# Kernel optimization log

Measured on AMD Instinct MI355X. Metric: run time of the kernel, lower is better.

Reference implementation:

```python
import jax, jax.numpy as jnp
import numpy as np

N_QUBITS = 10
DEPTH = 6


def _ry(theta):
    # RY(theta) = [[cos(t/2), -sin(t/2)], [sin(t/2), cos(t/2)]]
    c = jnp.cos(theta / 2)
    s = jnp.sin(theta / 2)
    return jnp.stack([jnp.stack([c, -s]), jnp.stack([s, c])]).astype(jnp.complex64)


def _rot(phi, theta, omega):
    # PennyLane Rot(phi, theta, omega) = RZ(omega) RY(theta) RZ(phi)
    c = jnp.cos(theta / 2)
    s = jnp.sin(theta / 2)
    ep = jnp.exp(-0.5j * (phi + omega).astype(jnp.complex64))
    em = jnp.exp(-0.5j * (phi - omega).astype(jnp.complex64))
    return jnp.stack([
        jnp.stack([ep * c, -jnp.conj(em) * s]),
        jnp.stack([em * s, jnp.conj(ep) * c]),
    ])


def _apply_1q(psi, U, w):
    # psi: (2,)*n statevector; apply 2x2 unitary U on qubit axis w
    psi = jnp.tensordot(U, psi, axes=([1], [w]))
    return jnp.moveaxis(psi, 0, w)


def _apply_cnot(psi, c, t):
    # flip target axis t on the control=1 slice of axis c
    psi = jnp.moveaxis(psi, (c, t), (0, 1))
    psi = jnp.concatenate([psi[:1], psi[1:, ::-1]], axis=0)
    return jnp.moveaxis(psi, (0, 1), (c, t))


def _circuit(angles, weights):
    """RY encoding + StronglyEntanglingLayers + PauliZ expvals. angles: (n,), weights: (depth, n, 3)."""
    n = N_QUBITS
    psi = jnp.zeros((2,) * n, jnp.complex64).at[(0,) * n].set(1.0)
    for i in range(n):
        psi = _apply_1q(psi, _ry(angles[i]), i)
    for l in range(DEPTH):
        for i in range(n):
            psi = _apply_1q(psi, _rot(weights[l, i, 0], weights[l, i, 1], weights[l, i, 2]), i)
        r = (l % (n - 1)) + 1  # default StronglyEntanglingLayers range schedule
        for i in range(n):
            psi = _apply_cnot(psi, i, (i + r) % n)
    p = psi.real ** 2 + psi.imag ** 2  # probabilities, shape (2,)*n
    exps = []
    for i in range(n):
        pm = jnp.moveaxis(p, i, 0).reshape(2, -1).sum(axis=1)
        exps.append(pm[0] - pm[1])  # <Z_i>
    return jnp.stack(exps)


def setup_inputs() -> dict:
    key = jax.random.key(0)
    ks = jax.random.split(key, 5)
    B, F, C = 8192, 1024, 10
    x = jax.random.normal(ks[0], (B, F), jnp.float32)
    W_proj = jax.random.normal(ks[1], (N_QUBITS, F), jnp.float32) / np.sqrt(F).astype(np.float32)
    weights = 0.01 * jax.random.normal(ks[2], (DEPTH, N_QUBITS, 3), jnp.float32)
    W_out = jax.random.normal(ks[3], (C, N_QUBITS), jnp.float32) / np.sqrt(N_QUBITS).astype(np.float32)
    b_out = 0.01 * jax.random.normal(ks[4], (C,), jnp.float32)
    return {"x": x, "W_proj": W_proj, "weights": weights, "W_out": W_out, "b_out": b_out}


def reference(x, W_proj, weights, W_out, b_out):
    # classical projection + angle encoding
    angles = jnp.tanh(x @ W_proj.T) * jnp.float32(np.pi / 2)  # (B, n_qubits)
    # batched exact statevector simulation of the VQC
    q = jax.vmap(_circuit, in_axes=(0, None))(angles, weights)  # (B, n_qubits)
    return q @ W_out.T + b_out  # (B, num_classes)
```

## Files before the change

### kernel.cpp

```cpp
#include <hip/hip_runtime.h>
#include <math.h>
#include <stdint.h>

#define NQ 10
#define DEPTH 6

typedef _Float16 f16x8 __attribute__((ext_vector_type(8)));
typedef float f32x4 __attribute__((ext_vector_type(4)));

typedef __attribute__((address_space(3))) unsigned int lds_u32;
typedef const __attribute__((address_space(1))) unsigned int glb_u32;

__device__ __forceinline__ void async_load16(const unsigned short* g, unsigned short* l) {
    __builtin_amdgcn_global_load_lds((glb_u32*)g, (lds_u32*)l, 16, 0, 0);
}

__device__ __forceinline__ void compute_gate(const float* __restrict__ weights,
                                             int idx, float* __restrict__ g) {
    float phi   = weights[idx * 3 + 0];
    float theta = weights[idx * 3 + 1];
    float omega = weights[idx * 3 + 2];
    float c = cosf(0.5f * theta), s = sinf(0.5f * theta);
    float ap = -0.5f * (phi + omega);
    float am = -0.5f * (phi - omega);
    float epr = cosf(ap), epi = sinf(ap);
    float emr = cosf(am), emi = sinf(am);
    g[0] =  epr * c;  g[1] =  epi * c;
    g[2] = -emr * s;  g[3] =  emi * s;
    g[4] =  emr * s;  g[5] =  emi * s;
    g[6] =  epr * c;  g[7] = -epi * c;
}

__global__ void prep_gates_kernel(const float* __restrict__ weights,
                                  float* __restrict__ gmat) {
    int idx = blockIdx.x * blockDim.x + threadIdx.x;
    if (idx >= DEPTH * NQ) return;
    compute_gate(weights, idx, gmat + idx * 8);
}

__device__ __forceinline__ void apply_1q_local(
    float (&ar)[16], float (&ai)[16], int q,
    float u00r, float u00i, float u01r, float u01i,
    float u10r, float u10i, float u11r, float u11i) {
#pragma unroll
    for (int j = 0; j < 16; ++j) {
        if ((j >> q) & 1) continue;
        int j1 = j | (1 << q);
        float a0r = ar[j],  a0i = ai[j];
        float a1r = ar[j1], a1i = ai[j1];
        ar[j]  = u00r*a0r - u00i*a0i + u01r*a1r - u01i*a1i;
        ai[j]  = u00r*a0i + u00i*a0r + u01r*a1i + u01i*a1r;
        ar[j1] = u10r*a0r - u10i*a0i + u11r*a1r - u11i*a1i;
        ai[j1] = u10r*a0i + u10i*a0r + u11r*a1i + u11i*a1r;
    }
}

__device__ __forceinline__ void apply_1q_lane(
    float (&ar)[16], float (&ai)[16], int q, int lane,
    float u00r, float u00i, float u01r, float u01i,
    float u10r, float u10i, float u11r, float u11i) {
    int  m  = 1 << (q - 4);
    bool hi = (lane >> (q - 4)) & 1;
    float car = hi ? u11r : u00r, cai = hi ? u11i : u00i;
    float cbr = hi ? u10r : u01r, cbi = hi ? u10i : u01i;
    float pr[16], pi[16];
#pragma unroll
    for (int j = 0; j < 16; ++j) pr[j] = __shfl_xor(ar[j], m, 64);
#pragma unroll
    for (int j = 0; j < 16; ++j) pi[j] = __shfl_xor(ai[j], m, 64);
#pragma unroll
    for (int j = 0; j < 16; ++j) {
        float mr = ar[j], mi = ai[j];
        ar[j] = car*mr - cai*mi + cbr*pr[j] - cbi*pi[j];
        ai[j] = car*mi + cai*mr + cbr*pi[j] + cbi*pr[j];
    }
}

__device__ __forceinline__ void cnot_gate(
    float (&ar)[16], float (&ai)[16], int c, int t, int lane) {
    if (c < 4 && t < 4) {
#pragma unroll
        for (int j = 0; j < 16; ++j) {
            if (((j >> c) & 1) && !((j >> t) & 1)) {
                int j1 = j | (1 << t);
                float tr = ar[j]; ar[j] = ar[j1]; ar[j1] = tr;
                float ti = ai[j]; ai[j] = ai[j1]; ai[j1] = ti;
            }
        }
    } else if (c < 4) {
        int m = 1 << (t - 4);
        float pr[16], pi[16];
#pragma unroll
        for (int j = 0; j < 16; ++j)
            if ((j >> c) & 1) pr[j] = __shfl_xor(ar[j], m, 64);
#pragma unroll
        for (int j = 0; j < 16; ++j)
            if ((j >> c) & 1) pi[j] = __shfl_xor(ai[j], m, 64);
#pragma unroll
        for (int j = 0; j < 16; ++j)
            if ((j >> c) & 1) { ar[j] = pr[j]; ai[j] = pi[j]; }
    } else if (t < 4) {
        bool cb = (lane >> (c - 4)) & 1;
#pragma unroll
        for (int j = 0; j < 16; ++j) {
            if (!((j >> t) & 1)) {
                int j1 = j | (1 << t);
                float lr = ar[j], li = ai[j], hr = ar[j1], hi2 = ai[j1];
                ar[j]  = cb ? hr : lr;  ai[j]  = cb ? hi2 : li;
                ar[j1] = cb ? lr : hr;  ai[j1] = cb ? li : hi2;
            }
        }
    } else {
        int  m  = 1 << (t - 4);
        bool cb = (lane >> (c - 4)) & 1;
        float pr[16], pi[16];
#pragma unroll
        for (int j = 0; j < 16; ++j) pr[j] = __shfl_xor(ar[j], m, 64);
#pragma unroll
        for (int j = 0; j < 16; ++j) pi[j] = __shfl_xor(ai[j], m, 64);
#pragma unroll
        for (int j = 0; j < 16; ++j) {
            ar[j] = cb ? pr[j] : ar[j];
            ai[j] = cb ? pi[j] : ai[j];
        }
    }
}

template <int R>
__device__ __forceinline__ void cnot_ring(float (&ar)[16], float (&ai)[16], int lane) {
#pragma unroll
    for (int i = 0; i < NQ; ++i) cnot_gate(ar, ai, i, (i + R) % NQ, lane);
}

template <int R>
__device__ __forceinline__ void cnot_ring_rev(float (&ar)[16], float (&ai)[16], int lane) {
#pragma unroll
    for (int i = NQ - 1; i >= 0; --i) cnot_gate(ar, ai, i, (i + R) % NQ, lane);
}

__device__ __forceinline__ void run_circuit(float (&ar)[16], float (&ai)[16],
                                            const float* __restrict__ gmat, int lane) {
    for (int l = 0; l < DEPTH; ++l) {
        const float* gl = gmat + l * (NQ * 8);
#pragma unroll
        for (int i = 0; i < NQ; ++i) {
            const float* g = gl + i * 8;
            float u00r = g[0], u00i = g[1], u01r = g[2], u01i = g[3];
            float u10r = g[4], u10i = g[5], u11r = g[6], u11i = g[7];
            if (i < 4)
                apply_1q_local(ar, ai, i, u00r,u00i,u01r,u01i,u10r,u10i,u11r,u11i);
            else
                apply_1q_lane(ar, ai, i, lane, u00r,u00i,u01r,u01i,u10r,u10i,u11r,u11i);
        }
        switch (l) {
            case 0: cnot_ring<1>(ar, ai, lane); break;
            case 1: cnot_ring<2>(ar, ai, lane); break;
            case 2: cnot_ring<3>(ar, ai, lane); break;
            case 3: cnot_ring<4>(ar, ai, lane); break;
            case 4: cnot_ring<5>(ar, ai, lane); break;
            default: cnot_ring<6>(ar, ai, lane); break;
        }
    }
}

__device__ __forceinline__ void run_circuit_T(float (&ar)[16], float (&ai)[16],
                                              const float* __restrict__ gmat, int lane) {
    for (int l = DEPTH - 1; l >= 0; --l) {
        switch (l) {
            case 0: cnot_ring_rev<1>(ar, ai, lane); break;
            case 1: cnot_ring_rev<2>(ar, ai, lane); break;
            case 2: cnot_ring_rev<3>(ar, ai, lane); break;
            case 3: cnot_ring_rev<4>(ar, ai, lane); break;
            case 4: cnot_ring_rev<5>(ar, ai, lane); break;
            default: cnot_ring_rev<6>(ar, ai, lane); break;
        }
        const float* gl = gmat + l * (NQ * 8);
#pragma unroll
        for (int i = 0; i < NQ; ++i) {
            const float* g = gl + i * 8;
            float u00r = g[0], u00i = g[1];
            float u01r = g[4], u01i = g[5];
            float u10r = g[2], u10i = g[3];
            float u11r = g[6], u11i = g[7];
            if (i < 4)
                apply_1q_local(ar, ai, i, u00r,u00i,u01r,u01i,u10r,u10i,u11r,u11i);
            else
                apply_1q_lane(ar, ai, i, lane, u00r,u00i,u01r,u01i,u10r,u10i,u11r,u11i);
        }
    }
}

__device__ __forceinline__ float wave_sum(float v) {
#pragma unroll
    for (int m = 1; m < 64; m <<= 1) v += __shfl_xor(v, m, 64);
    return v;
}

__device__ __forceinline__ void proj_v_body(
    const float* __restrict__ x, const float* __restrict__ Wproj,
    _Float16* __restrict__ V, int b, int lane) {
    const float4* xb4 = (const float4*)(x + (size_t)b * 1024);
    const float4* W4  = (const float4*)Wproj;
    float acc[NQ];
#pragma unroll
    for (int q = 0; q < NQ; ++q) acc[q] = 0.f;
#pragma unroll
    for (int k4 = 0; k4 < 4; ++k4) {
        float4 xv = xb4[k4 * 64 + lane];
#pragma unroll
        for (int q = 0; q < NQ; ++q) {
            float4 wv = W4[q * 256 + k4 * 64 + lane];
            acc[q] = fmaf(xv.x, wv.x, acc[q]);
            acc[q] = fmaf(xv.y, wv.y, acc[q]);
            acc[q] = fmaf(xv.z, wv.z, acc[q]);
            acc[q] = fmaf(xv.w, wv.w, acc[q]);
        }
    }
#pragma unroll
    for (int q = 0; q < NQ; ++q) acc[q] = wave_sum(acc[q]);

    float cq[NQ], sq[NQ];
#pragma unroll
    for (int q = 0; q < NQ; ++q) {
        float ang = tanhf(acc[q]) * 1.57079632679489662f;
        cq[q] = cosf(0.5f * ang);
        sq[q] = sinf(0.5f * ang);
    }
    float laneprod = 1.f;
#pragma unroll
    for (int q = 4; q < NQ; ++q)
        laneprod *= ((lane >> (q - 4)) & 1) ? sq[q] : cq[q];

    unsigned int buf[8];
#pragma unroll
    for (int jj = 0; jj < 8; ++jj) {
        unsigned short h2[2];
#pragma unroll
        for (int c = 0; c < 2; ++c) {
            int j = jj * 2 + c;
            float p = laneprod;
#pragma unroll
            for (int q = 0; q < 4; ++q) p *= ((j >> q) & 1) ? sq[q] : cq[q];
            h2[c] = __builtin_bit_cast(unsigned short, (_Float16)p);
        }
        buf[jj] = (unsigned int)h2[0] | ((unsigned int)h2[1] << 16);
    }
    uint4* dst = (uint4*)(V + (size_t)b * 1024 + 16 * lane);
    uint4 v0; v0.x = buf[0]; v0.y = buf[1]; v0.z = buf[2]; v0.w = buf[3];
    uint4 v1; v1.x = buf[4]; v1.y = buf[5]; v1.z = buf[6]; v1.w = buf[7];
    dst[0] = v0; dst[1] = v1;
}

__global__ __launch_bounds__(256) void basis_proj_kernel(
    const float* __restrict__ weights, _Float16* __restrict__ Bt,
    const float* __restrict__ x, const float* __restrict__ Wproj,
    _Float16* __restrict__ V, int B) {
    __shared__ float gmat_s[DEPTH * NQ * 8];
    int tid  = threadIdx.x;
    int lane = tid & 63;
    int w    = tid >> 6;

    if (blockIdx.x < 256) {
        if (tid < DEPTH * NQ) compute_gate(weights, tid, gmat_s + tid * 8);
        __syncthreads();

        int g = blockIdx.x * 4 + w;
        float ar[16], ai[16];
#pragma unroll
        for (int jj = 0; jj < 16; ++jj) {
            ar[jj] = (lane == (g >> 4) && jj == (g & 15)) ? 1.f : 0.f;
            ai[jj] = 0.f;
        }
        run_circuit_T(ar, ai, gmat_s, lane);

        unsigned int bufr[8], bufi[8];
#pragma unroll
        for (int jj = 0; jj < 8; ++jj) {
            unsigned short r0 = __builtin_bit_cast(unsigned short, (_Float16)ar[2*jj]);
            unsigned short r1 = __builtin_bit_cast(unsigned short, (_Float16)ar[2*jj+1]);
            unsigned short i0 = __builtin_bit_cast(unsigned short, (_Float16)ai[2*jj]);
            unsigned short i1 = __builtin_bit_cast(unsigned short, (_Float16)ai[2*jj+1]);
            bufr[jj] = (unsigned int)r0 | ((unsigned int)r1 << 16);
            bufi[jj] = (unsigned int)i0 | ((unsigned int)i1 << 16);
        }
        uint4* dre = (uint4*)((unsigned short*)Bt + (size_t)(2*g)     * 1024 + 16 * lane);
        uint4* dim = (uint4*)((unsigned short*)Bt + (size_t)(2*g + 1) * 1024 + 16 * lane);
        uint4 v;
        v.x = bufr[0]; v.y = bufr[1]; v.z = bufr[2]; v.w = bufr[3]; dre[0] = v;
        v.x = bufr[4]; v.y = bufr[5]; v.z = bufr[6]; v.w = bufr[7]; dre[1] = v;
        v.x = bufi[0]; v.y = bufi[1]; v.z = bufi[2]; v.w = bufi[3]; dim[0] = v;
        v.x = bufi[4]; v.y = bufi[5]; v.z = bufi[6]; v.w = bufi[7]; dim[1] = v;
    } else {
        int b = (blockIdx.x - 256) * 4 + w;
        if (b < B) proj_v_body(x, Wproj, V, b, lane);
    }
}

#define STAGE(buf, kt_) do {                                                        \
    unsigned short* As_ = lds_s + (buf) * 32768;                                    \
    unsigned short* Bs_ = As_ + 16384;                                              \
    _Pragma("unroll")                                                               \
    for (int r_ = 0; r_ < 4; ++r_) {                                                \
        int s_   = w * 4 + r_;                                                      \
        int row_ = s_ * 8 + srow;                                                   \
        async_load16(A  + (size_t)(m0 + row_) * 1024 + (kt_) * 64 + schnk * 8,      \
                     As_ + s_ * 512);                                               \
        async_load16(Bt + (size_t)(n0 + row_) * 1024 + (kt_) * 64 + schnk * 8,      \
                     Bs_ + s_ * 512);                                               \
    }                                                                               \
} while (0)

__global__ __launch_bounds__(512, 2) void gemm_fused_kernel(
    const unsigned short* __restrict__ A,
    const unsigned short* __restrict__ Bt,
    float* __restrict__ Zpart) {
    __shared__ __align__(16) unsigned short lds_s[2 * 32768];
    int tid  = threadIdx.x;
    int lane = tid & 63;
    int w    = tid >> 6;
    int wm   = w >> 2;
    int wn   = w & 3;
    int by   = blockIdx.x & 7;
    int bx   = blockIdx.x >> 3;
    int m0   = bx * 256;
    int n0   = by * 256;
    int quad = lane >> 4;
    int lrow = lane & 15;
    int srow  = (lane >> 3);
    int schnk = (lane & 7) ^ srow;

    f32x4 acc[8][4];
#pragma unroll
    for (int mi = 0; mi < 8; ++mi)
#pragma unroll
        for (int ni = 0; ni < 4; ++ni)
            acc[mi][ni] = (f32x4){0.f, 0.f, 0.f, 0.f};

    STAGE(0, 0);

#pragma unroll 2
    for (int kt = 0; kt < 16; ++kt) {
        int cur = kt & 1;
        if (kt < 15) {
            STAGE(cur ^ 1, kt + 1);
            asm volatile("s_waitcnt vmcnt(8)" ::: "memory");
        } else {
            asm volatile("s_waitcnt vmcnt(0)" ::: "memory");
        }
        __builtin_amdgcn_s_barrier();
        asm volatile("" ::: "memory");
        const unsigned short* As_ = lds_s + cur * 32768;
        const unsigned short* Bs_ = As_ + 16384;
#pragma unroll
        for (int kk = 0; kk < 2; ++kk) {
            int cx = (kk * 4 + quad) ^ (lrow & 7);
            f16x8 bf[4];
#pragma unroll
            for (int ni = 0; ni < 4; ++ni)
                bf[ni] = *(const f16x8*)(Bs_ + (wn * 64 + ni * 16 + lrow) * 64 + cx * 8);
            __builtin_amdgcn_s_setprio(1);
#pragma unroll
            for (int mi = 0; mi < 8; ++mi) {
                f16x8 af = *(const f16x8*)(As_ + (wm * 128 + mi * 16 + lrow) * 64 + cx * 8);
#pragma unroll
                for (int ni = 0; ni < 4; ++ni)
                    acc[mi][ni] = __builtin_amdgcn_mfma_f32_16x16x32_f16(
                        af, bf[ni], acc[mi][ni], 0, 0, 0);
            }
            __builtin_amdgcn_s_setprio(0);
        }
        asm volatile("" ::: "memory");
        __builtin_amdgcn_s_barrier();
    }

    float* Zs = (float*)lds_s;
    int nbl  = wn >> 1;
    int half = wn & 1;
#pragma unroll
    for (int mi = 0; mi < 8; ++mi) {
#pragma unroll
        for (int r = 0; r < 4; ++r) {
            float p0 = acc[mi][0][r] * acc[mi][0][r];
            float p1 = acc[mi][1][r] * acc[mi][1][r];
            float p2 = acc[mi][2][r] * acc[mi][2][r];
            float p3 = acc[mi][3][r] * acc[mi][3][r];
            float t0 = (p0 + p1) + (p2 + p3);
            float t3 = (p0 - p1) + (p2 - p3);
            float t4 = (p0 + p1) - (p2 + p3);
            t0 += __shfl_xor(t0, 1, 64);
            t3 += __shfl_xor(t3, 1, 64);
            t4 += __shfl_xor(t4, 1, 64);
            float u2 = __shfl_xor(t0, 2, 64);
            float ap = t0 + u2;
            float am = (lane & 2) ? u2 - t0 : t0 - u2;
            t3 += __shfl_xor(t3, 2, 64);
            t4 += __shfl_xor(t4, 2, 64);
            float u4  = __shfl_xor(ap, 4, 64);
            float bpp = ap + u4;
            float bpm = (lane & 4) ? u4 - ap : ap - u4;
            float bmp = am + __shfl_xor(am, 4, 64);
            t3 += __shfl_xor(t3, 4, 64);
            t4 += __shfl_xor(t4, 4, 64);
            float u8 = __shfl_xor(bpp, 8, 64);
            float T  = bpp + u8;
            float Z2 = (lane & 8) ? u8 - bpp : bpp - u8;
            float Z1 = bpm + __shfl_xor(bpm, 8, 64);
            float Z0 = bmp + __shfl_xor(bmp, 8, 64);
            t3 += __shfl_xor(t3, 8, 64);
            t4 += __shfl_xor(t4, 8, 64);
            if (lrow == 0) {
                int row = wm * 128 + mi * 16 + quad * 4 + r;
                float* z = Zs + ((size_t)(nbl * 2 + half) * 256 + row) * 9;
                z[0] = T;  z[1] = Z0; z[2] = Z1; z[3] = Z2;
                z[4] = t3; z[5] = t4;
            }
        }
    }
    __syncthreads();
    {
        int row  = tid >> 1, part = tid & 1;
#pragma unroll
        for (int nb = 0; nb < 2; ++nb) {
            const float* za = Zs + ((size_t)(nb * 2 + 0) * 256 + row) * 9;
            const float* zb = Zs + ((size_t)(nb * 2 + 1) * 256 + row) * 9;
            float o[4];
            if (part == 0) {
                o[0] = za[0] + zb[0];
                o[1] = za[1] + zb[1];
                o[2] = za[2] + zb[2];
                o[3] = za[3] + zb[3];
            } else {
                o[0] = za[4] + zb[4];
                o[1] = za[5] + zb[5];
                o[2] = za[0] - zb[0];
                o[3] = 0.f;
            }
            float4 v = {o[0], o[1], o[2], o[3]};
            *(float4*)(Zpart + ((size_t)(m0 + row) * 16 + (by * 2 + nb)) * 8 + part * 4) = v;
        }
    }
}

__global__ __launch_bounds__(256) void combine_head_kernel(
    const float* __restrict__ Zpart, const float* __restrict__ Wout,
    const float* __restrict__ bout, float* __restrict__ out, int B) {
    int lane = threadIdx.x & 63;
    int wid  = threadIdx.x >> 6;
    int b    = blockIdx.x * 4 + wid;
    if (b >= B) return;

    float z[8];
    if (lane < 16) {
        const float4* p = (const float4*)(Zpart + ((size_t)b * 16 + lane) * 8);
        float4 a = p[0], c = p[1];
        z[0]=a.x; z[1]=a.y; z[2]=a.z; z[3]=a.w; z[4]=c.x; z[5]=c.y; z[6]=c.z; z[7]=c.w;
    } else {
#pragma unroll
        for (int i = 0; i < 8; ++i) z[i] = 0.f;
    }
    float Zq[NQ];
#pragma unroll
    for (int q = 0; q < 6; ++q) {
        float v = z[q + 1];
        v += __shfl_xor(v, 1, 64);
        v += __shfl_xor(v, 2, 64);
        v += __shfl_xor(v, 4, 64);
        v += __shfl_xor(v, 8, 64);
        Zq[q] = v;
    }
    {
        float T = z[0];
        float u1 = __shfl_xor(T, 1, 64);
        float P  = T + u1;
        float M  = (lane & 1) ? u1 - T : T - u1;
        float u2 = __shfl_xor(P, 2, 64);
        float PP = P + u2;
        float PM = (lane & 2) ? u2 - P : P - u2;
        float MP = M + __shfl_xor(M, 2, 64);
        float u4  = __shfl_xor(PP, 4, 64);
        float PPP = PP + u4;
        float PPM = (lane & 4) ? u4 - PP : PP - u4;
        float PMP = PM + __shfl_xor(PM, 4, 64);
        float MPP = MP + __shfl_xor(MP, 4, 64);
        float u8 = __shfl_xor(PPP, 8, 64);
        Zq[9] = (lane & 8) ? u8 - PPP : PPP - u8;
        Zq[8] = PPM + __shfl_xor(PPM, 8, 64);
        Zq[7] = PMP + __shfl_xor(PMP, 8, 64);
        Zq[6] = MPP + __shfl_xor(MPP, 8, 64);
    }
    if (lane < NQ) {
        float o = bout[lane];
#pragma unroll
        for (int q = 0; q < NQ; ++q) o = fmaf(Zq[q], Wout[lane * NQ + q], o);
        out[(size_t)b * NQ + lane] = o;
    }
}

__global__ __launch_bounds__(256) void vqc_kernel(
    const float* __restrict__ x, const float* __restrict__ Wproj,
    const float* __restrict__ gmat, const float* __restrict__ Wout,
    const float* __restrict__ bout, float* __restrict__ out, int B) {
    int lane = threadIdx.x & 63;
    int wid  = threadIdx.x >> 6;
    int b    = blockIdx.x * 4 + wid;
    if (b >= B) return;

    const float* xb = x + (size_t)b * 1024;
    float acc[NQ];
#pragma unroll
    for (int q = 0; q < NQ; ++q) acc[q] = 0.f;
#pragma unroll
    for (int k = 0; k < 16; ++k) {
        float xv = xb[k * 64 + lane];
#pragma unroll
        for (int q = 0; q < NQ; ++q)
            acc[q] = fmaf(xv, Wproj[q * 1024 + k * 64 + lane], acc[q]);
    }
#pragma unroll
    for (int q = 0; q < NQ; ++q) acc[q] = wave_sum(acc[q]);

    float cq[NQ], sq[NQ];
#pragma unroll
    for (int q = 0; q < NQ; ++q) {
        float ang = tanhf(acc[q]) * 1.57079632679489662f;
        cq[q] = cosf(0.5f * ang);
        sq[q] = sinf(0.5f * ang);
    }
    float laneprod = 1.f;
#pragma unroll
    for (int q = 4; q < NQ; ++q)
        laneprod *= ((lane >> (q - 4)) & 1) ? sq[q] : cq[q];
    float ar[16], ai[16];
#pragma unroll
    for (int j = 0; j < 16; ++j) {
        float p = laneprod;
#pragma unroll
        for (int q = 0; q < 4; ++q) p *= ((j >> q) & 1) ? sq[q] : cq[q];
        ar[j] = p; ai[j] = 0.f;
    }
    run_circuit(ar, ai, gmat, lane);

    float T = 0.f, S[4] = {0.f, 0.f, 0.f, 0.f};
#pragma unroll
    for (int j = 0; j < 16; ++j) {
        float p = ar[j] * ar[j] + ai[j] * ai[j];
        T += p;
#pragma unroll
        for (int q = 0; q < 4; ++q) S[q] += ((j >> q) & 1) ? -p : p;
    }
    float Zq[NQ];
#pragma unroll
    for (int q = 0; q < 4; ++q) Zq[q] = S[q];
#pragma unroll
    for (int q = 4; q < NQ; ++q) Zq[q] = ((lane >> (q - 4)) & 1) ? -T : T;
#pragma unroll
    for (int q = 0; q < NQ; ++q) Zq[q] = wave_sum(Zq[q]);
    if (lane < NQ) {
        float o = bout[lane];
#pragma unroll
        for (int q = 0; q < NQ; ++q) o = fmaf(Zq[q], Wout[lane * NQ + q], o);
        out[(size_t)b * NQ + lane] = o;
    }
}

extern "C" void kernel_launch(void* const* d_in, const int* in_sizes, int n_in,
                              void* d_out, int out_size, void* d_ws, size_t ws_size,
                              hipStream_t stream) {
    const float* x       = (const float*)d_in[0];
    const float* Wproj   = (const float*)d_in[1];
    const float* weights = (const float*)d_in[2];
    const float* Wout    = (const float*)d_in[3];
    const float* bout    = (const float*)d_in[4];
    float* out = (float*)d_out;
    int B = in_sizes[0] / 1024;

    char* ws = (char*)d_ws;
    size_t off_Bt = 4096;
    size_t off_V  = off_Bt + (size_t)2048 * 1024 * 2;
    size_t off_Z  = off_V  + (size_t)B * 1024 * 2;
    size_t need   = off_Z  + (size_t)B * 16 * 8 * 4;

    if (ws_size >= need && (B % 256) == 0) {
        _Float16* Bt = (_Float16*)(ws + off_Bt);
        _Float16* V  = (_Float16*)(ws + off_V);
        float*  Zprt = (float*)(ws + off_Z);

        basis_proj_kernel<<<256 + B / 4, 256, 0, stream>>>(weights, Bt, x, Wproj, V, B);
        gemm_fused_kernel<<<(B / 256) * 8, 512, 0, stream>>>(
            (const unsigned short*)V, (const unsigned short*)Bt, Zprt);
        combine_head_kernel<<<B / 4, 256, 0, stream>>>(Zprt, Wout, bout, out, B);
    } else {
        float* gmat = (float*)ws;
        prep_gates_kernel<<<1, 64, 0, stream>>>(weights, gmat);
        vqc_kernel<<<(B + 3) / 4, 256, 0, stream>>>(x, Wproj, gmat, Wout, bout, out, B);
    }
}
```

Measured before the change: 160.7 us.

## Restructure GEMM mainloop into 4-stage K=32 pipeline with split A/B staging

Replaces the double-buffered K=64 tile loop with a four-buffer, K=32-per-stage pipeline that prefetches three stages ahead. Each iteration is split into two halves: the A-stage load is issued during the first MFMA half and the B-stage load during the second, with barriers and explicit lgkmcnt waits between them. LDS swizzling and per-thread load mapping are changed to fit 32-column rows. This aims to hide global-to-LDS latency better and interleave LDS reads with MFMA issue, at the cost of more barriers per K step and a more fragile wait-count scheme.

```diff
diff --git a/kernel.cpp b/kernel.cpp
--- a/kernel.cpp
+++ b/kernel.cpp
@@ -296,17 +296,11 @@
     }
 }
 
-#define STAGE(buf, kt_) do {                                                        \
-    unsigned short* As_ = lds_s + (buf) * 32768;                                    \
-    unsigned short* Bs_ = As_ + 16384;                                              \
+#define STG(dst_, src_, kt_) do {                                                   \
     _Pragma("unroll")                                                               \
-    for (int r_ = 0; r_ < 4; ++r_) {                                                \
-        int s_   = w * 4 + r_;                                                      \
-        int row_ = s_ * 8 + srow;                                                   \
-        async_load16(A  + (size_t)(m0 + row_) * 1024 + (kt_) * 64 + schnk * 8,      \
-                     As_ + s_ * 512);                                               \
-        async_load16(Bt + (size_t)(n0 + row_) * 1024 + (kt_) * 64 + schnk * 8,      \
-                     Bs_ + s_ * 512);                                               \
+    for (int s_ = 0; s_ < 2; ++s_) {                                                \
+        async_load16(src_ + (size_t)(s_ * 128 + srow) * 1024 + (kt_) * 32 + scg * 8,\
+                     dst_ + s_ * 4096 + w * 512);                                   \
     }                                                                               \
 } while (0)
 
@@ -314,7 +308,7 @@
     const unsigned short* __restrict__ A,
     const unsigned short* __restrict__ Bt,
     float* __restrict__ Zpart) {
-    __shared__ __align__(16) unsigned short lds_s[2 * 32768];
+    __shared__ __align__(16) unsigned short lds_s[4 * 16384];
     int tid  = threadIdx.x;
     int lane = tid & 63;
     int w    = tid >> 6;
@@ -326,8 +320,11 @@
     int n0   = by * 256;
     int quad = lane >> 4;
     int lrow = lane & 15;
-    int srow  = (lane >> 3);
-    int schnk = (lane & 7) ^ srow;
+    int csw  = (quad ^ ((lrow >> 1) & 3)) * 8;
+    int srow = tid >> 2;
+    int scg  = (tid & 3) ^ ((srow >> 1) & 3);
+    const unsigned short* Abase = A  + (size_t)m0 * 1024;
+    const unsigned short* Bbase = Bt + (size_t)n0 * 1024;
 
     f32x4 acc[8][4];
 #pragma unroll
@@ -336,40 +333,62 @@
         for (int ni = 0; ni < 4; ++ni)
             acc[mi][ni] = (f32x4){0.f, 0.f, 0.f, 0.f};
 
-    STAGE(0, 0);
-
-#pragma unroll 2
-    for (int kt = 0; kt < 16; ++kt) {
-        int cur = kt & 1;
-        if (kt < 15) {
-            STAGE(cur ^ 1, kt + 1);
+    STG(lds_s + 0 * 16384,        Abase, 0);
+    STG(lds_s + 0 * 16384 + 8192, Bbase, 0);
+    STG(lds_s + 1 * 16384,        Abase, 1);
+    STG(lds_s + 1 * 16384 + 8192, Bbase, 1);
+    STG(lds_s + 2 * 16384,        Abase, 2);
+    STG(lds_s + 2 * 16384 + 8192, Bbase, 2);
+    asm volatile("s_waitcnt vmcnt(8)" ::: "memory");
+    __builtin_amdgcn_s_barrier();
+
+    int rowA = wm * 128 + lrow;
+    int rowB = wn * 64  + lrow;
+
+    for (int t = 0; t < 32; ++t) {
+        const unsigned short* bufA = lds_s + (t & 3) * 16384;
+        const unsigned short* bufB = bufA + 8192;
+        unsigned short* nbuf = lds_s + ((t + 3) & 3) * 16384;
+        f16x8 af[4], bf[4];
+#pragma unroll
+        for (int i = 0; i < 4; ++i)
+            af[i] = *(const f16x8*)(bufA + (rowA + i * 16) * 32 + csw);
+#pragma unroll
+        for (int i = 0; i < 4; ++i)
+            bf[i] = *(const f16x8*)(bufB + (rowB + i * 16) * 32 + csw);
+        if (t < 29) STG(nbuf, Abase, t + 3);
+        __builtin_amdgcn_s_barrier();
+        asm volatile("s_waitcnt lgkmcnt(0)" ::: "memory");
+        __builtin_amdgcn_sched_barrier(0);
+        __builtin_amdgcn_s_setprio(1);
+#pragma unroll
+        for (int mi = 0; mi < 4; ++mi)
+#pragma unroll
+            for (int ni = 0; ni < 4; ++ni)
+                acc[mi][ni] = __builtin_amdgcn_mfma_f32_16x16x32_f16(
+                    af[mi], bf[ni], acc[mi][ni], 0, 0, 0);
+        __builtin_amdgcn_s_setprio(0);
+        __builtin_amdgcn_s_barrier();
+#pragma unroll
+        for (int i = 0; i < 4; ++i)
+            af[i] = *(const f16x8*)(bufA + (rowA + 64 + i * 16) * 32 + csw);
+        if (t < 29) {
+            STG(nbuf + 8192, Bbase, t + 3);
             asm volatile("s_waitcnt vmcnt(8)" ::: "memory");
         } else {
             asm volatile("s_waitcnt vmcnt(0)" ::: "memory");
         }
         __builtin_amdgcn_s_barrier();
-        asm volatile("" ::: "memory");
-        const unsigned short* As_ = lds_s + cur * 32768;
-        const unsigned short* Bs_ = As_ + 16384;
-#pragma unroll
-        for (int kk = 0; kk < 2; ++kk) {
-            int cx = (kk * 4 + quad) ^ (lrow & 7);
-            f16x8 bf[4];
+        asm volatile("s_waitcnt lgkmcnt(0)" ::: "memory");
+        __builtin_amdgcn_sched_barrier(0);
+        __builtin_amdgcn_s_setprio(1);
+#pragma unroll
+        for (int mi = 0; mi < 4; ++mi)
 #pragma unroll
             for (int ni = 0; ni < 4; ++ni)
-                bf[ni] = *(const f16x8*)(Bs_ + (wn * 64 + ni * 16 + lrow) * 64 + cx * 8);
-            __builtin_amdgcn_s_setprio(1);
-#pragma unroll
-            for (int mi = 0; mi < 8; ++mi) {
-                f16x8 af = *(const f16x8*)(As_ + (wm * 128 + mi * 16 + lrow) * 64 + cx * 8);
-#pragma unroll
-                for (int ni = 0; ni < 4; ++ni)
-                    acc[mi][ni] = __builtin_amdgcn_mfma_f32_16x16x32_f16(
-                        af, bf[ni], acc[mi][ni], 0, 0, 0);
-            }
-            __builtin_amdgcn_s_setprio(0);
-        }
-        asm volatile("" ::: "memory");
+                acc[mi + 4][ni] = __builtin_amdgcn_mfma_f32_16x16x32_f16(
+                    af[mi], bf[ni], acc[mi + 4][ni], 0, 0, 0);
+        __builtin_amdgcn_s_setprio(0);
         __builtin_amdgcn_s_barrier();
     }
 
```

Result: no change. 163.6 us (+1.8%).
